# Kernel tuning notes

Measured on AMD Instinct MI355X. Metric: run time of the kernel, lower is better.

Reference implementation:

```python
import jax, jax.numpy as jnp
import numpy as np

SMOOTH = 1e-3
EPS = 1e-12


def setup_inputs() -> dict:
    key = jax.random.key(0)
    k1, k2, k3 = jax.random.split(key, 3)
    pred = jax.random.normal(k1, (1, 16, 384, 384), dtype=jnp.float32)
    labels = jax.random.randint(k2, (1, 16, 384, 384), 0, 2, dtype=jnp.int32)
    # stand-in for create_table_neighbour_code_to_surface_area((1,1,1)): 256-entry LUT
    area = jax.random.uniform(k3, (256,), dtype=jnp.float32) * 2.0
    return {"pred": pred, "labels": labels, "area": area}


def _corners(x2):
    # x2: (B, 2, Y+2, X+2) zero-padded slice pair -> (B, 8, (Y+1)*(X+1))
    # corner index k = dz*4 + dy*2 + dx, matching torch unfold(kernel=(2,2), padding=1)
    B, _, Yp, Xp = x2.shape
    Y, X = Yp - 1, Xp - 1
    cs = [x2[:, dz, dy:dy + Y, dx:dx + X]
          for dz in (0, 1) for dy in (0, 1) for dx in (0, 1)]
    return jnp.stack(cs, axis=1).reshape(B, 8, Y * X)


def _surface_dice(pred_sig, labels, area, smooth):
    B, Z, Y, X = pred_sig.shape
    # bases[i, k] = bit k of code i  (== [c=='1' for c in f'{i:08b}'[::-1]])
    bits = jnp.arange(8, dtype=jnp.int32)
    bases = ((jnp.arange(256, dtype=jnp.int32)[:, None] >> bits[None, :]) & 1).astype(jnp.float32)  # (256,8)
    n_bits = bases.sum(1)  # (256,) popcount

    # blank zero slices on both z ends + the unfold's zero padding in y/x
    Pp = jnp.pad(pred_sig, ((0, 0), (1, 1), (1, 1), (1, 1)))
    Lp = jnp.pad(labels.astype(jnp.int32), ((0, 0), (1, 1), (1, 1), (1, 1)))

    def pair(carry, i):
        num, den, vol = carry
        pz = jax.lax.dynamic_slice(Pp, (0, i, 0, 0), (B, 2, Y + 2, X + 2))
        lz = jax.lax.dynamic_slice(Lp, (0, i, 0, 0), (B, 2, Y + 2, X + 2))
        pc = _corners(pz)                      # (B, 8, Np) float
        lc = _corners(lz)                      # (B, 8, Np) int32
        byte = jnp.left_shift(lc, bits[None, :, None]).sum(axis=1)  # (B, Np) label corner code

        # basis_weights = 1 - mean_k (pc_k - bases_ik)^2, expanded so the
        # (B,256,8,Np) broadcast is never materialized
        sp2 = jnp.sum(pc * pc, axis=1)                       # (B, Np)
        cross = jnp.einsum('bkn,ik->bin', pc, bases)         # (B, 256, Np)
        bw = 1.0 - (sp2[:, None, :] + n_bits[None, :, None] - 2.0 * cross) / 8.0

        pred_byte = jnp.argmax(bw, axis=1)                   # (B, Np)
        pred_area = area[pred_byte]                          # (B, Np)
        label_area = area[byte]                              # (B, Np)
        pw = jnp.take_along_axis(bw, byte[:, None, :], axis=1)[:, 0]  # (B, Np)

        # binary_cross_entropy(unfolded_pred, unfolded_labels) per element
        lf = lc.astype(jnp.float32)
        logp = jnp.log(jnp.maximum(pc, EPS))
        log1mp = jnp.log(jnp.maximum(1.0 - pc, EPS))
        bce = -(lf * logp + (1.0 - lf) * log1mp)             # (B, 8, Np)
        interior = (byte == 0) | (byte == 255)               # (B, Np)
        v = jnp.where(interior[:, None, :], bce, 0.0).mean((1, 2))

        inter = jnp.sum(pw * label_area, axis=1)
        return (num + 2.0 * inter,
                den + label_area.sum(1) + pred_area.sum(1),
                vol + v), None

    init = (jnp.zeros((B,), jnp.float32), jnp.zeros((B,), jnp.float32), jnp.zeros((B,), jnp.float32))
    (num, den, vol), _ = jax.lax.scan(pair, init, jnp.arange(Z + 1))
    dice = 1.0 - (num + smooth) / (den + smooth)
    return dice.mean() + vol.mean()


def reference(pred, labels, area):
    return _surface_dice(jax.nn.sigmoid(pred), labels, area, SMOOTH)
```

## Files before the change

### kernel.cpp

```cpp
#include <hip/hip_runtime.h>
#include <math.h>

constexpr int ZN = 16, YN = 384, XN = 384;
constexpr int NZ = 17, NY = 385, NX = 385;
constexpr int NP = NY * NX;
constexpr int TOTAL = NZ * NP;

constexpr int NBLK = 1280;

__global__ __launch_bounds__(256) void sd_main(
        const float* __restrict__ pred,
        const int*   __restrict__ labels,
        const float* __restrict__ area,
        float*       __restrict__ partial)
{
    __shared__ float s_area[256];
    s_area[threadIdx.x] = area[threadIdx.x];
    __syncthreads();

    float num = 0.f, den = 0.f, vol = 0.f;
    const int stride = gridDim.x * blockDim.x;
    for (int i = blockIdx.x * blockDim.x + threadIdx.x; i < TOTAL; i += stride) {
        const int z   = i / NP;
        const int rem = i - z * NP;
        const int y   = rem / NX;
        const int x   = rem - y * NX;

        float pc[8];
        float lf[8];
        int byte = 0, pbyte = 0;
#pragma unroll
        for (int k = 0; k < 8; ++k) {
            const int dz = k >> 2, dy = (k >> 1) & 1, dx = k & 1;
            const int zz = z + dz - 1, yy = y + dy - 1, xx = x + dx - 1;
            const bool in = ((unsigned)zz < (unsigned)ZN) &
                            ((unsigned)yy < (unsigned)YN) &
                            ((unsigned)xx < (unsigned)XN);
            float p = 0.f; int l = 0;
            if (in) {
                const int off = (zz * YN + yy) * XN + xx;
                p = pred[off];
                l = labels[off];
            }
            const float s = in ? __fdividef(1.f, 1.f + __expf(-p)) : 0.f;
            pc[k] = s;
            lf[k] = (float)l;
            byte  |= l << k;
            pbyte |= (int)(in && (p > 0.f)) << k;
        }

        float sq = 0.f;
#pragma unroll
        for (int k = 0; k < 8; ++k) { const float d = pc[k] - lf[k]; sq += d * d; }
        const float pw = 1.f - sq * 0.125f;

        const float la = s_area[byte];
        const float pa = s_area[pbyte];
        num += 2.f * pw * la;
        den += la + pa;

        if (byte == 0 || byte == 255) {
            float b = 0.f;
#pragma unroll
            for (int k = 0; k < 8; ++k) {
                const float t = (lf[k] != 0.f) ? __logf(fmaxf(pc[k], 1e-12f))
                                               : __logf(fmaxf(1.f - pc[k], 1e-12f));
                b -= t;
            }
            vol += b;
        }
    }

#pragma unroll
    for (int off = 32; off > 0; off >>= 1) {
        num += __shfl_down(num, off);
        den += __shfl_down(den, off);
        vol += __shfl_down(vol, off);
    }
    __shared__ float sn[4], sd_[4], sv[4];
    const int lane = threadIdx.x & 63, w = threadIdx.x >> 6;
    if (lane == 0) { sn[w] = num; sd_[w] = den; sv[w] = vol; }
    __syncthreads();
    if (threadIdx.x == 0) {
        partial[blockIdx.x]            = sn[0] + sn[1] + sn[2] + sn[3];
        partial[NBLK + blockIdx.x]     = sd_[0] + sd_[1] + sd_[2] + sd_[3];
        partial[2 * NBLK + blockIdx.x] = sv[0] + sv[1] + sv[2] + sv[3];
    }
}

__global__ __launch_bounds__(256) void sd_final(
        const float* __restrict__ partial, float* __restrict__ out)
{
    double n = 0.0, d = 0.0, v = 0.0;
    for (int b = threadIdx.x; b < NBLK; b += 256) {
        n += (double)partial[b];
        d += (double)partial[NBLK + b];
        v += (double)partial[2 * NBLK + b];
    }
#pragma unroll
    for (int off = 32; off > 0; off >>= 1) {
        n += __shfl_down(n, off);
        d += __shfl_down(d, off);
        v += __shfl_down(v, off);
    }
    __shared__ double sn[4], sd_[4], sv[4];
    const int lane = threadIdx.x & 63, w = threadIdx.x >> 6;
    if (lane == 0) { sn[w] = n; sd_[w] = d; sv[w] = v; }
    __syncthreads();
    if (threadIdx.x == 0) {
        const double num = sn[0] + sn[1] + sn[2] + sn[3];
        const double den = sd_[0] + sd_[1] + sd_[2] + sd_[3];
        const double vol = (sv[0] + sv[1] + sv[2] + sv[3]) / (8.0 * (double)NP);
        const double dice = 1.0 - (num + 1e-3) / (den + 1e-3);
        out[0] = (float)(dice + vol);
    }
}

extern "C" void kernel_launch(void* const* d_in, const int* in_sizes, int n_in,
                              void* d_out, int out_size, void* d_ws, size_t ws_size,
                              hipStream_t stream)
{
    const float* pred   = (const float*)d_in[0];
    const int*   labels = (const int*)d_in[1];
    const float* area   = (const float*)d_in[2];
    float* out     = (float*)d_out;
    float* partial = (float*)d_ws;

    sd_main<<<NBLK, 256, 0, stream>>>(pred, labels, area, partial);
    sd_final<<<1, 256, 0, stream>>>(partial, out);
}
```

Measured before the change: 99.60 us.

## Map one wavefront per output row and share column corners via lane shuffles

Assigns each 64-lane wavefront one (z,y) row of corner nodes. Each lane loads and applies sigmoid to only 4 voxels (one column of the 2x2 z/y neighbourhood) and gets the neighbouring column from the adjacent lane via shuffles, with a carry across 64-wide chunks. This replaces 8 loads, 8 sigmoids and a divide-based index decomposition per node. The area LUT is permuted in shared memory so it can be indexed by interleaved column codes. The aim is less redundant global traffic and transcendental work, at the cost of shuffle overhead and an extra tail node handled on lane 0.

```diff
diff --git a/kernel.cpp b/kernel.cpp
--- a/kernel.cpp
+++ b/kernel.cpp
@@ -4,9 +4,8 @@
 constexpr int ZN = 16, YN = 384, XN = 384;
 constexpr int NZ = 17, NY = 385, NX = 385;
 constexpr int NP = NY * NX;
-constexpr int TOTAL = NZ * NP;
-
-constexpr int NBLK = 1280;
+constexpr int NROWS = NZ * NY;
+constexpr int BLOCKS = 1637;
 
 __global__ __launch_bounds__(256) void sd_main(
         const float* __restrict__ pred,
@@ -15,59 +14,96 @@
         float*       __restrict__ partial)
 {
     __shared__ float s_area[256];
-    s_area[threadIdx.x] = area[threadIdx.x];
+    {
+        const int t = threadIdx.x;
+        const int own = t >> 4, prv = t & 15;
+        int code = 0;
+#pragma unroll
+        for (int r = 0; r < 4; ++r)
+            code |= (((prv >> r) & 1) << (2 * r)) | (((own >> r) & 1) << (2 * r + 1));
+        s_area[t] = area[code];
+    }
     __syncthreads();
 
+    const int lane = threadIdx.x & 63;
+    const int wid  = blockIdx.x * 4 + (threadIdx.x >> 6);
+
     float num = 0.f, den = 0.f, vol = 0.f;
-    const int stride = gridDim.x * blockDim.x;
-    for (int i = blockIdx.x * blockDim.x + threadIdx.x; i < TOTAL; i += stride) {
-        const int z   = i / NP;
-        const int rem = i - z * NP;
-        const int y   = rem / NX;
-        const int x   = rem - y * NX;
 
-        float pc[8];
-        float lf[8];
-        int byte = 0, pbyte = 0;
+    if (wid < NROWS) {
+        const int z = wid / NY;
+        const int y = wid - z * NY;
+
+        bool rv[4]; int base[4];
 #pragma unroll
-        for (int k = 0; k < 8; ++k) {
-            const int dz = k >> 2, dy = (k >> 1) & 1, dx = k & 1;
-            const int zz = z + dz - 1, yy = y + dy - 1, xx = x + dx - 1;
-            const bool in = ((unsigned)zz < (unsigned)ZN) &
-                            ((unsigned)yy < (unsigned)YN) &
-                            ((unsigned)xx < (unsigned)XN);
-            float p = 0.f; int l = 0;
-            if (in) {
-                const int off = (zz * YN + yy) * XN + xx;
-                p = pred[off];
-                l = labels[off];
-            }
-            const float s = in ? __fdividef(1.f, 1.f + __expf(-p)) : 0.f;
-            pc[k] = s;
-            lf[k] = (float)l;
-            byte  |= l << k;
-            pbyte |= (int)(in && (p > 0.f)) << k;
+        for (int r = 0; r < 4; ++r) {
+            const int zz = z - 1 + (r >> 1);
+            const int yy = y - 1 + (r & 1);
+            rv[r]   = ((unsigned)zz < (unsigned)ZN) & ((unsigned)yy < (unsigned)YN);
+            base[r] = (zz * YN + yy) * XN;
         }
 
-        float sq = 0.f;
+        float cs[4] = {0.f, 0.f, 0.f, 0.f};
+        int   cb = 0;
+
+        auto do_node = [&](const float s[4], int LP, const float ps[4], int PLP) {
+            const int idxL = ((LP & 15) << 4) | (PLP & 15);
+            const int idxP = (LP & 0xF0) | (PLP >> 4);
+            const float la = s_area[idxL];
+            const float pa = s_area[idxP];
+            float u[8];
+            float sq = 0.f;
 #pragma unroll
-        for (int k = 0; k < 8; ++k) { const float d = pc[k] - lf[k]; sq += d * d; }
-        const float pw = 1.f - sq * 0.125f;
+            for (int r = 0; r < 4; ++r) {
+                const float u0 = ((PLP >> r) & 1) ? ps[r] : 1.f - ps[r];
+                const float u1 = ((LP  >> r) & 1) ? s[r]  : 1.f - s[r];
+                u[2 * r] = u0; u[2 * r + 1] = u1;
+                const float d0 = 1.f - u0, d1 = 1.f - u1;
+                sq += d0 * d0 + d1 * d1;
+            }
+            const float pw = 1.f - sq * 0.125f;
+            num += 2.f * pw * la;
+            den += la + pa;
+            if (idxL == 0 || idxL == 255) {
+                float b = 0.f;
+#pragma unroll
+                for (int k = 0; k < 8; ++k)
+                    b += __logf(fmaxf(u[k], 1e-12f));
+                vol -= b;
+            }
+        };
 
-        const float la = s_area[byte];
-        const float pa = s_area[pbyte];
-        num += 2.f * pw * la;
-        den += la + pa;
-
-        if (byte == 0 || byte == 255) {
-            float b = 0.f;
+        for (int chunk = 0; chunk < 6; ++chunk) {
+            const int x = chunk * 64 + lane;
+            float s[4]; int LP = 0;
 #pragma unroll
-            for (int k = 0; k < 8; ++k) {
-                const float t = (lf[k] != 0.f) ? __logf(fmaxf(pc[k], 1e-12f))
-                                               : __logf(fmaxf(1.f - pc[k], 1e-12f));
-                b -= t;
+            for (int r = 0; r < 4; ++r) {
+                if (rv[r]) {
+                    const float p = pred[base[r] + x];
+                    const int   l = labels[base[r] + x];
+                    s[r] = __fdividef(1.f, 1.f + __expf(-p));
+                    LP  |= (l << r) | ((int)(p > 0.f) << (r + 4));
+                } else {
+                    s[r] = 0.f;
+                }
             }
-            vol += b;
+            float ps[4]; int PLP;
+#pragma unroll
+            for (int r = 0; r < 4; ++r) ps[r] = __shfl_up(s[r], 1);
+            PLP = __shfl_up(LP, 1);
+            if (lane == 0) {
+#pragma unroll
+                for (int r = 0; r < 4; ++r) ps[r] = cs[r];
+                PLP = cb;
+            }
+            do_node(s, LP, ps, PLP);
+#pragma unroll
+            for (int r = 0; r < 4; ++r) cs[r] = __shfl(s[r], 63);
+            cb = __shfl(LP, 63);
+        }
+        if (lane == 0) {
+            const float zs[4] = {0.f, 0.f, 0.f, 0.f};
+            do_node(zs, 0, cs, cb);
         }
     }
 
@@ -78,13 +114,13 @@
         vol += __shfl_down(vol, off);
     }
     __shared__ float sn[4], sd_[4], sv[4];
-    const int lane = threadIdx.x & 63, w = threadIdx.x >> 6;
+    const int w = threadIdx.x >> 6;
     if (lane == 0) { sn[w] = num; sd_[w] = den; sv[w] = vol; }
     __syncthreads();
     if (threadIdx.x == 0) {
-        partial[blockIdx.x]            = sn[0] + sn[1] + sn[2] + sn[3];
-        partial[NBLK + blockIdx.x]     = sd_[0] + sd_[1] + sd_[2] + sd_[3];
-        partial[2 * NBLK + blockIdx.x] = sv[0] + sv[1] + sv[2] + sv[3];
+        partial[blockIdx.x]              = sn[0] + sn[1] + sn[2] + sn[3];
+        partial[BLOCKS + blockIdx.x]     = sd_[0] + sd_[1] + sd_[2] + sd_[3];
+        partial[2 * BLOCKS + blockIdx.x] = sv[0] + sv[1] + sv[2] + sv[3];
     }
 }
 
@@ -92,10 +128,10 @@
         const float* __restrict__ partial, float* __restrict__ out)
 {
     double n = 0.0, d = 0.0, v = 0.0;
-    for (int b = threadIdx.x; b < NBLK; b += 256) {
+    for (int b = threadIdx.x; b < BLOCKS; b += 256) {
         n += (double)partial[b];
-        d += (double)partial[NBLK + b];
-        v += (double)partial[2 * NBLK + b];
+        d += (double)partial[BLOCKS + b];
+        v += (double)partial[2 * BLOCKS + b];
     }
 #pragma unroll
     for (int off = 32; off > 0; off >>= 1) {
@@ -126,6 +162,6 @@
     float* out     = (float*)d_out;
     float* partial = (float*)d_ws;
 
-    sd_main<<<NBLK, 256, 0, stream>>>(pred, labels, area, partial);
+    sd_main<<<BLOCKS, 256, 0, stream>>>(pred, labels, area, partial);
     sd_final<<<1, 256, 0, stream>>>(partial, out);
 }
```

Result: faster. 89.07 us (-10.6%).
